# Performance work log

Measured on AMD Instinct MI355X. Metric: run time of the kernel, lower is better.

Reference implementation:

```python
import jax, jax.numpy as jnp
import numpy as np

B, N, M = 4, 2048, 2048
DIM, DIM_KEYS, DIM_OUT = 512, 512, 512
HEADS, DIM_HEAD = 8, 64
INNER = HEADS * DIM_HEAD


def setup_inputs() -> dict:
    key = jax.random.key(0)
    ks = jax.random.split(key, 8)
    x = jax.random.normal(ks[0], (B, N, DIM), dtype=jnp.float32)
    context = jax.random.normal(ks[1], (B, M, DIM_KEYS), dtype=jnp.float32)
    Wq = jax.random.normal(ks[2], (DIM, INNER), dtype=jnp.float32) / np.sqrt(DIM)
    Wkv = jax.random.normal(ks[3], (DIM_KEYS, 2 * INNER), dtype=jnp.float32) / np.sqrt(DIM_KEYS)
    null_k = jax.random.normal(ks[4], (DIM_HEAD,), dtype=jnp.float32)
    null_v = jax.random.normal(ks[5], (DIM_HEAD,), dtype=jnp.float32)
    Wout = jax.random.normal(ks[6], (INNER, DIM_OUT), dtype=jnp.float32) / np.sqrt(INNER)
    bout = jnp.zeros((DIM_OUT,), dtype=jnp.float32)
    return {"x": x, "context": context, "Wq": Wq, "Wkv": Wkv,
            "null_k": null_k, "null_v": null_v, "Wout": Wout, "bout": bout}


def reference(x, context, Wq, Wkv, null_k, null_v, Wout, bout):
    b = x.shape[0]
    scale = DIM_HEAD ** (-0.5)
    q = x @ Wq                      # [b, n, inner]
    kv = context @ Wkv              # [b, m, 2*inner]
    k, v = jnp.split(kv, 2, axis=-1)
    # [b, h, n, d]
    q = q.reshape(b, -1, HEADS, DIM_HEAD).transpose(0, 2, 1, 3)
    k = k.reshape(b, -1, HEADS, DIM_HEAD).transpose(0, 2, 1, 3)
    v = v.reshape(b, -1, HEADS, DIM_HEAD).transpose(0, 2, 1, 3)
    # prepend null key/value token: [b, h, 1, d]
    nk = jnp.broadcast_to(null_k, (b, HEADS, 1, DIM_HEAD))
    nv = jnp.broadcast_to(null_v, (b, HEADS, 1, DIM_HEAD))
    k = jnp.concatenate((nk, k), axis=-2)  # [b, h, m+1, d]
    v = jnp.concatenate((nv, v), axis=-2)
    q = jnp.tanh(q)
    k = jnp.tanh(k)
    sim = jnp.einsum('bhid,bhjd->bhij', q, k) * scale  # [b, h, n, m+1]
    attn = jax.nn.softmax(sim, axis=-1)
    out = jnp.einsum('bhij,bhjd->bhid', attn, v)       # [b, h, n, d]
    out = out.transpose(0, 2, 1, 3).reshape(b, -1, INNER)  # [b, n, inner]
    return out @ Wout + bout
```

## Files before the change

kernel.cpp:

```cpp
#include <hip/hip_runtime.h>
#include <hip/hip_bf16.h>
#include <stdint.h>

#define B_    4
#define N_    2048
#define M_    2048
#define DIMX  512
#define INNER 512
#define H_    8
#define DH    64
#define MK    2049
#define MKP   2112

#define QSCALE  0.18033688011f
#define SM_BIAS -11.5415605f

using u16 = unsigned short;
using u32 = unsigned int;

typedef __attribute__((ext_vector_type(8))) short short8;
typedef __attribute__((ext_vector_type(4))) float f32x4;

#if defined(__has_builtin)
# if __has_builtin(__builtin_amdgcn_exp2f)
#  define EXP2(x) __builtin_amdgcn_exp2f(x)
# endif
#endif
#ifndef EXP2
# define EXP2(x) exp2f(x)
#endif

__device__ __forceinline__ u16 bfc(float f){
  __hip_bfloat16 h = __float2bfloat16(f);
  return *reinterpret_cast<u16*>(&h);
}
__device__ __forceinline__ u32 bfpk(float lo, float hi){
  return (u32)bfc(lo) | ((u32)bfc(hi) << 16);
}
__device__ __forceinline__ u32 bfpk_tr(float lo, float hi){
  union { float f; u32 u; } a, b; a.f = lo; b.f = hi;
  return (a.u >> 16) | (b.u & 0xffff0000u);
}

__global__ __launch_bounds__(256) void prep(
    const float* __restrict__ x, const float* __restrict__ ctx,
    const float* __restrict__ Wq, const float* __restrict__ Wkv,
    const float* __restrict__ Wout,
    const float* __restrict__ nk, const float* __restrict__ nv,
    u16* __restrict__ xb, u16* __restrict__ cb,
    u16* __restrict__ Wqt, u16* __restrict__ Wkvt, u16* __restrict__ Woutt,
    u16* __restrict__ kb, u16* __restrict__ vt)
{
  const int bid = blockIdx.x;
  if (bid < 4096){
    const float* in = (bid < 2048) ? x : ctx;
    u16* out        = (bid < 2048) ? xb : cb;
    const int i = (bid & 2047) * 256 + threadIdx.x;
    float4 a = ((const float4*)in)[i*2];
    float4 b = ((const float4*)in)[i*2+1];
    uint4 t;
    t.x = bfpk(a.x, a.y); t.y = bfpk(a.z, a.w);
    t.z = bfpk(b.x, b.y); t.w = bfpk(b.z, b.w);
    ((uint4*)out)[i] = t;
    return;
  }
  if (bid >= 4480){
    const int i = (bid - 4480) * 256 + threadIdx.x;
    const int d = i & 63, bh = i >> 6;
    kb[((size_t)bh * MKP + 2048) * DH + d] = bfc(tanhf(nk[d]));
    vt[((size_t)bh * DH + d) * MKP + 2048] = bfc(nv[d]);
    return;
  }
  const int tt = bid - 4096;
  const int z  = tt >> 7;
  const int rem = tt & 127;
  const int cx = rem & 15, ry = rem >> 4;
  const float* in = (z == 0) ? Wq : (z == 1) ? Wkv : Wout;
  u16* out        = (z == 0) ? Wqt : (z == 1) ? Wkvt : Woutt;
  const int C     = (z == 1) ? 1024 : 512;
  const int R     = 512;
  if (cx * 64 >= C) return;

  __shared__ float tl[64][65];
  const int t = threadIdx.x;
  const int c0 = cx * 64, r0 = ry * 64;
  const int col = t & 63, rb = t >> 6;
  #pragma unroll
  for (int j = 0; j < 16; ++j){
    const int row = rb + j*4;
    tl[row][col] = in[(size_t)(r0 + row) * C + c0 + col];
  }
  __syncthreads();
  #pragma unroll
  for (int j = 0; j < 16; ++j){
    const int orow = rb + j*4;
    out[(size_t)(c0 + orow) * R + r0 + col] = bfc(tl[col][orow]);
  }
}

#define PROJ_COMPUTE(bi)                                                      \
  {                                                                           \
    short8 af[4], bf[4];                                                      \
    _Pragma("unroll")                                                         \
    for (int m = 0; m < 4; ++m){                                              \
      const int row = wr + m*16 + c;                                          \
      af[m] = *(const short8*)((char*)At[bi] + row*64 + ((g ^ ((row>>1)&3)) << 4)); \
    }                                                                         \
    _Pragma("unroll")                                                         \
    for (int n = 0; n < 4; ++n){                                              \
      const int row = wc + n*16 + c;                                          \
      bf[n] = *(const short8*)((char*)Bl[bi] + row*64 + ((g ^ ((row>>1)&3)) << 4)); \
    }                                                                         \
    __builtin_amdgcn_s_setprio(1);                                            \
    _Pragma("unroll")                                                         \
    for (int m = 0; m < 4; ++m)                                               \
      _Pragma("unroll")                                                       \
      for (int n = 0; n < 4; ++n)                                             \
        acc[m][n] = __builtin_amdgcn_mfma_f32_16x16x32_bf16(af[m], bf[n], acc[m][n], 0, 0, 0); \
    __builtin_amdgcn_s_setprio(0);                                            \
  }

__global__ __launch_bounds__(256, 3) void fused_proj(
    const u16* __restrict__ xb, const u16* __restrict__ cb,
    const u16* __restrict__ Wqt, const u16* __restrict__ Wkvt,
    u16* __restrict__ qb, u16* __restrict__ kb, u16* __restrict__ vt)
{
  __shared__ __align__(16) short At[2][128*32];
  __shared__ __align__(16) short Bl[2][128*32];

  const int flat = blockIdx.x;
  const int tile = (flat & 7) * 96 + (flat >> 3);
  const bool isq = tile < 256;
  const int lt   = isq ? tile : tile - 256;
  const int gx   = isq ? 4 : 8;
  const int row0 = (lt / gx) * 128, col0 = (lt % gx) * 128;
  const u16* A  = isq ? xb : cb;
  const u16* Bt = isq ? Wqt : Wkvt;

  const int tid = threadIdx.x;
  const int w = tid >> 6, lane = tid & 63;
  const int c = lane & 15, g = lane >> 4;
  const int wr = (w >> 1) * 64, wc = (w & 1) * 64;

  f32x4 acc[4][4] = {};

  const int srow = tid >> 1, sj = (tid & 1) * 2;
  const int swz0 = ((sj  ) ^ ((srow >> 1) & 3)) << 4;
  const int swz1 = ((sj+1) ^ ((srow >> 1) & 3)) << 4;

  const u16* asrc = A  + (size_t)(row0 + srow) * DIMX + sj*8;
  const u16* bsrc = Bt + (size_t)(col0 + srow) * DIMX + sj*8;

  uint4 aA0, aA1, bA0, bA1;
  uint4 aB0, aB1, bB0, bB1;

  aA0 = ((const uint4*)asrc)[0];        aA1 = ((const uint4*)asrc)[1];
  bA0 = ((const uint4*)bsrc)[0];        bA1 = ((const uint4*)bsrc)[1];
  aB0 = ((const uint4*)(asrc + 32))[0]; aB1 = ((const uint4*)(asrc + 32))[1];
  bB0 = ((const uint4*)(bsrc + 32))[0]; bB1 = ((const uint4*)(bsrc + 32))[1];
  *(uint4*)((char*)At[0] + srow*64 + swz0) = aA0;
  *(uint4*)((char*)At[0] + srow*64 + swz1) = aA1;
  *(uint4*)((char*)Bl[0] + srow*64 + swz0) = bA0;
  *(uint4*)((char*)Bl[0] + srow*64 + swz1) = bA1;

  for (int kk = 0; kk < 16; kk += 2){
    __syncthreads();
    if (kk + 2 < 16){
      const u16* an = asrc + (kk+2)*32;
      const u16* bn = bsrc + (kk+2)*32;
      aA0 = ((const uint4*)an)[0]; aA1 = ((const uint4*)an)[1];
      bA0 = ((const uint4*)bn)[0]; bA1 = ((const uint4*)bn)[1];
    }
    PROJ_COMPUTE(0);
    *(uint4*)((char*)At[1] + srow*64 + swz0) = aB0;
    *(uint4*)((char*)At[1] + srow*64 + swz1) = aB1;
    *(uint4*)((char*)Bl[1] + srow*64 + swz0) = bB0;
    *(uint4*)((char*)Bl[1] + srow*64 + swz1) = bB1;

    __syncthreads();
    if (kk + 3 < 16){
      const u16* an = asrc + (kk+3)*32;
      const u16* bn = bsrc + (kk+3)*32;
      aB0 = ((const uint4*)an)[0]; aB1 = ((const uint4*)an)[1];
      bB0 = ((const uint4*)bn)[0]; bB1 = ((const uint4*)bn)[1];
    }
    PROJ_COMPUTE(1);
    if (kk + 2 < 16){
      *(uint4*)((char*)At[0] + srow*64 + swz0) = aA0;
      *(uint4*)((char*)At[0] + srow*64 + swz1) = aA1;
      *(uint4*)((char*)Bl[0] + srow*64 + swz0) = bA0;
      *(uint4*)((char*)Bl[0] + srow*64 + swz1) = bA1;
    }
  }

  #pragma unroll
  for (int m = 0; m < 4; ++m){
    #pragma unroll
    for (int n = 0; n < 4; ++n){
      const int R0  = row0 + wr + m*16 + g*4;
      const int col = col0 + wc + n*16 + c;
      if (isq){
        #pragma unroll
        for (int rr = 0; rr < 4; ++rr)
          qb[(size_t)(R0 + rr) * INNER + col] = bfc(tanhf(acc[m][n][rr]) * QSCALE);
      } else {
        const int bidx = R0 >> 11, mm = R0 & 2047;
        if (col < INNER){
          const int h = col >> 6, d = col & 63;
          #pragma unroll
          for (int rr = 0; rr < 4; ++rr)
            kb[((size_t)(bidx*H_ + h) * MKP + mm + rr) * DH + d] =
                bfc(tanhf(acc[m][n][rr]));
        } else {
          const int cc = col - INNER;
          const int h = cc >> 6, d = cc & 63;
          uint2 o;
          o.x = bfpk(acc[m][n][0], acc[m][n][1]);
          o.y = bfpk(acc[m][n][2], acc[m][n][3]);
          *(uint2*)(vt + ((size_t)(bidx*H_ + h) * DH + d) * MKP + mm) = o;
        }
      }
    }
  }
}

__global__ __launch_bounds__(256, 3) void mgemm_out(
    const u16* __restrict__ A, const u16* __restrict__ Bt,
    float* __restrict__ Cf, const float* __restrict__ bias)
{
  __shared__ __align__(16) short At[2][128*32];
  __shared__ __align__(16) short Bl[2][64*32];

  const int flat = blockIdx.x;
  const int tile = (flat & 7) * 64 + (flat >> 3);
  const int row0 = (tile >> 3) * 128, col0 = (tile & 7) * 64;

  const int tid = threadIdx.x;
  const int w = tid >> 6, lane = tid & 63;
  const int c = lane & 15, g = lane >> 4;
  const int wr = (w >> 1) * 64, wc = (w & 1) * 32;

  f32x4 acc[4][2] = {};

  const int srow = tid >> 1, sj = (tid & 1) * 2;
  const int swz0 = ((sj  ) ^ ((srow >> 1) & 3)) << 4;
  const int swz1 = ((sj+1) ^ ((srow >> 1) & 3)) << 4;
  const int brow = tid >> 2, bch = tid & 3;
  const int bswz = (bch ^ ((brow >> 1) & 3)) << 4;

  const u16* asrc = A  + (size_t)(row0 + srow) * INNER + sj*8;
  const u16* bsrc = Bt + (size_t)(col0 + brow) * INNER + bch*8;

  uint4 aA0, aA1, bA0;
  uint4 aB0, aB1, bB0;

  aA0 = ((const uint4*)asrc)[0];        aA1 = ((const uint4*)asrc)[1];
  bA0 = *(const uint4*)bsrc;
  aB0 = ((const uint4*)(asrc + 32))[0]; aB1 = ((const uint4*)(asrc + 32))[1];
  bB0 = *(const uint4*)(bsrc + 32);
  *(uint4*)((char*)At[0] + srow*64 + swz0) = aA0;
  *(uint4*)((char*)At[0] + srow*64 + swz1) = aA1;
  *(uint4*)((char*)Bl[0] + brow*64 + bswz) = bA0;

  for (int kk = 0; kk < 16; kk += 2){
    __syncthreads();
    if (kk + 2 < 16){
      const u16* an = asrc + (kk+2)*32;
      aA0 = ((const uint4*)an)[0]; aA1 = ((const uint4*)an)[1];
      bA0 = *(const uint4*)(bsrc + (kk+2)*32);
    }
    {
      short8 af[4], bf[2];
      #pragma unroll
      for (int m = 0; m < 4; ++m){
        const int row = wr + m*16 + c;
        af[m] = *(const short8*)((char*)At[0] + row*64 + ((g ^ ((row>>1)&3)) << 4));
      }
      #pragma unroll
      for (int n = 0; n < 2; ++n){
        const int row = wc + n*16 + c;
        bf[n] = *(const short8*)((char*)Bl[0] + row*64 + ((g ^ ((row>>1)&3)) << 4));
      }
      __builtin_amdgcn_s_setprio(1);
      #pragma unroll
      for (int m = 0; m < 4; ++m)
        #pragma unroll
        for (int n = 0; n < 2; ++n)
          acc[m][n] = __builtin_amdgcn_mfma_f32_16x16x32_bf16(af[m], bf[n], acc[m][n], 0, 0, 0);
      __builtin_amdgcn_s_setprio(0);
    }
    *(uint4*)((char*)At[1] + srow*64 + swz0) = aB0;
    *(uint4*)((char*)At[1] + srow*64 + swz1) = aB1;
    *(uint4*)((char*)Bl[1] + brow*64 + bswz) = bB0;

    __syncthreads();
    if (kk + 3 < 16){
      const u16* an = asrc + (kk+3)*32;
      aB0 = ((const uint4*)an)[0]; aB1 = ((const uint4*)an)[1];
      bB0 = *(const uint4*)(bsrc + (kk+3)*32);
    }
    {
      short8 af[4], bf[2];
      #pragma unroll
      for (int m = 0; m < 4; ++m){
        const int row = wr + m*16 + c;
        af[m] = *(const short8*)((char*)At[1] + row*64 + ((g ^ ((row>>1)&3)) << 4));
      }
      #pragma unroll
      for (int n = 0; n < 2; ++n){
        const int row = wc + n*16 + c;
        bf[n] = *(const short8*)((char*)Bl[1] + row*64 + ((g ^ ((row>>1)&3)) << 4));
      }
      __builtin_amdgcn_s_setprio(1);
      #pragma unroll
      for (int m = 0; m < 4; ++m)
        #pragma unroll
        for (int n = 0; n < 2; ++n)
          acc[m][n] = __builtin_amdgcn_mfma_f32_16x16x32_bf16(af[m], bf[n], acc[m][n], 0, 0, 0);
      __builtin_amdgcn_s_setprio(0);
    }
    if (kk + 2 < 16){
      *(uint4*)((char*)At[0] + srow*64 + swz0) = aA0;
      *(uint4*)((char*)At[0] + srow*64 + swz1) = aA1;
      *(uint4*)((char*)Bl[0] + brow*64 + bswz) = bA0;
    }
  }

  #pragma unroll
  for (int m = 0; m < 4; ++m){
    #pragma unroll
    for (int n = 0; n < 2; ++n){
      #pragma unroll
      for (int rr = 0; rr < 4; ++rr){
        const int R = row0 + wr + m*16 + g*4 + rr;
        const int col = col0 + wc + n*16 + c;
        Cf[(size_t)R * 512 + col] = acc[m][n][rr] + bias[col];
      }
    }
  }
}

__global__ __launch_bounds__(256) void attn_mfma(
    const u16* __restrict__ qb, const u16* __restrict__ kb,
    const u16* __restrict__ vt, u16* __restrict__ aob)
{
  __shared__ __align__(16) short Kl[2][64*64];
  __shared__ __align__(16) short Vl[2][64*64];
  __shared__ __align__(16) short Pl[4][32*64];

  const int tid  = threadIdx.x;
  const int w    = tid >> 6;
  const int lane = tid & 63;
  const int c    = lane & 15;
  const int g    = lane >> 4;
  const int bh   = blockIdx.y, b = bh >> 3, h = bh & 7;
  const int qbase = blockIdx.x * 128 + w * 32;
  const int xr   = (c & 7) << 4;

  short8 qf[2][2];
  #pragma unroll
  for (int u = 0; u < 2; ++u){
    const u16* qrow = qb + ((size_t)(b*N_) + qbase + u*16 + c) * INNER + h * DH;
    qf[u][0] = *(const short8*)(qrow + g*8);
    qf[u][1] = *(const short8*)(qrow + 32 + g*8);
  }

  f32x4 o[2][4] = {};
  f32x4 lacc[2] = {};
  const short8 ones = {0x3F80,0x3F80,0x3F80,0x3F80,0x3F80,0x3F80,0x3F80,0x3F80};

  const u16* kbase = kb + (size_t)bh * MKP * DH;
  const u16* vbase = vt + (size_t)bh * DH * MKP;
  const int srow = tid >> 2, sch = (tid & 3) * 2;
  const int swz0 = ((sch  ) ^ (srow & 7)) << 4;
  const int swz1 = ((sch+1) ^ (srow & 7)) << 4;

  uint4 rk0, rk1, rv0, rv1;
  {
    const u16* ksrc = kbase + (size_t)srow * DH + sch*8;
    rk0 = ((const uint4*)ksrc)[0]; rk1 = ((const uint4*)ksrc)[1];
    const u16* vsrc = vbase + (size_t)srow * MKP + sch*8;
    rv0 = ((const uint4*)vsrc)[0]; rv1 = ((const uint4*)vsrc)[1];
  }
  *(uint4*)((char*)Kl[0] + srow*128 + swz0) = rk0;
  *(uint4*)((char*)Kl[0] + srow*128 + swz1) = rk1;
  *(uint4*)((char*)Vl[0] + srow*128 + swz0) = rv0;
  *(uint4*)((char*)Vl[0] + srow*128 + swz1) = rv1;

  int cur = 0;
  for (int kt = 0; kt < 33; ++kt){
    __syncthreads();
    if (kt < 32){
      const u16* ksrc = kbase + (size_t)((kt+1)*64 + srow) * DH + sch*8;
      rk0 = ((const uint4*)ksrc)[0]; rk1 = ((const uint4*)ksrc)[1];
      const u16* vsrc = vbase + (size_t)srow * MKP + (kt+1)*64 + sch*8;
      rv0 = ((const uint4*)vsrc)[0]; rv1 = ((const uint4*)vsrc)[1];
    }

    const char* Kc = (const char*)Kl[cur];
    const char* Vc = (const char*)Vl[cur];
    char*       Pw = (char*)Pl + w*4096;

    f32x4 sv[2][4];
    __builtin_amdgcn_s_setprio(1);
    #pragma unroll
    for (int s = 0; s < 4; ++s){
      const int row = s*16 + c;
      short8 kf0 = *(const short8*)(Kc + row*128 + ((     g*16) ^ xr));
      short8 kf1 = *(const short8*)(Kc + row*128 + ((64 + g*16) ^ xr));
      f32x4 a0 = {SM_BIAS, SM_BIAS, SM_BIAS, SM_BIAS};
      f32x4 a1 = {SM_BIAS, SM_BIAS, SM_BIAS, SM_BIAS};
      a0 = __builtin_amdgcn_mfma_f32_16x16x32_bf16(kf0, qf[0][0], a0, 0, 0, 0);
      a1 = __builtin_amdgcn_mfma_f32_16x16x32_bf16(kf0, qf[1][0], a1, 0, 0, 0);
      a0 = __builtin_amdgcn_mfma_f32_16x16x32_bf16(kf1, qf[0][1], a0, 0, 0, 0);
      a1 = __builtin_amdgcn_mfma_f32_16x16x32_bf16(kf1, qf[1][1], a1, 0, 0, 0);
      sv[0][s] = a0; sv[1][s] = a1;
    }
    __builtin_amdgcn_s_setprio(0);

    if (kt == 32){
      #pragma unroll
      for (int u = 0; u < 2; ++u)
        #pragma unroll
        for (int s = 0; s < 4; ++s)
          #pragma unroll
          for (int r = 0; r < 4; ++r)
            if (s | r) sv[u][s][r] = -1e30f;
      if (g){ sv[0][0][0] = -1e30f; sv[1][0][0] = -1e30f; }
    }

    #pragma unroll
    for (int u = 0; u < 2; ++u){
      #pragma unroll
      for (int s = 0; s < 4; ++s){
        const float p0 = EXP2(sv[u][s][0]);
        const float p1 = EXP2(sv[u][s][1]);
        const float p2 = EXP2(sv[u][s][2]);
        const float p3 = EXP2(sv[u][s][3]);
        uint2 pk;
        pk.x = bfpk_tr(p0, p1);
        pk.y = bfpk_tr(p2, p3);
        *(uint2*)(Pw + (u*16 + c)*128
                  + ((((2*s + (g>>1)) ^ (c&7)) << 4) | ((g&1)*8))) = pk;
      }
    }

    __builtin_amdgcn_s_setprio(1);
    #pragma unroll
    for (int hh = 0; hh < 2; ++hh){
      short8 pf0 = *(const short8*)(Pw + (     c)*128 + (((hh*4 + g) ^ (c&7)) << 4));
      short8 pf1 = *(const short8*)(Pw + (16 + c)*128 + (((hh*4 + g) ^ (c&7)) << 4));
      lacc[0] = __builtin_amdgcn_mfma_f32_16x16x32_bf16(pf0, ones, lacc[0], 0, 0, 0);
      lacc[1] = __builtin_amdgcn_mfma_f32_16x16x32_bf16(pf1, ones, lacc[1], 0, 0, 0);
      #pragma unroll
      for (int D = 0; D < 4; ++D){
        short8 vf = *(const short8*)(Vc + (D*16 + c)*128 + ((hh*64 + g*16) ^ xr));
        o[0][D] = __builtin_amdgcn_mfma_f32_16x16x32_bf16(pf0, vf, o[0][D], 0, 0, 0);
        o[1][D] = __builtin_amdgcn_mfma_f32_16x16x32_bf16(pf1, vf, o[1][D], 0, 0, 0);
      }
    }
    __builtin_amdgcn_s_setprio(0);

    if (kt < 32){
      char* Kn = (char*)Kl[cur ^ 1];
      char* Vn = (char*)Vl[cur ^ 1];
      *(uint4*)(Kn + srow*128 + swz0) = rk0;
      *(uint4*)(Kn + srow*128 + swz1) = rk1;
      *(uint4*)(Vn + srow*128 + swz0) = rv0;
      *(uint4*)(Vn + srow*128 + swz1) = rv1;
      cur ^= 1;
    }
  }

  #pragma unroll
  for (int u = 0; u < 2; ++u){
    #pragma unroll
    for (int r = 0; r < 4; ++r){
      const float ir = 1.f / lacc[u][r];
      const size_t nrow = (size_t)(b*N_) + qbase + u*16 + g*4 + r;
      #pragma unroll
      for (int D = 0; D < 4; ++D)
        aob[nrow * INNER + h*DH + D*16 + c] = bfc(o[u][D][r] * ir);
    }
  }
}

extern "C" void kernel_launch(void* const* d_in, const int* in_sizes, int n_in,
                              void* d_out, int out_size, void* d_ws, size_t ws_size,
                              hipStream_t stream)
{
  const float* x    = (const float*)d_in[0];
  const float* ctx  = (const float*)d_in[1];
  const float* Wq   = (const float*)d_in[2];
  const float* Wkv  = (const float*)d_in[3];
  const float* nk   = (const float*)d_in[4];
  const float* nv   = (const float*)d_in[5];
  const float* Wout = (const float*)d_in[6];
  const float* bout = (const float*)d_in[7];
  float* out = (float*)d_out;

  char* ws = (char*)d_ws;
  u16* xb    = (u16*)(ws);
  u16* cb    = (u16*)(ws +  8388608);
  u16* qb    = (u16*)(ws + 16777216);
  u16* kbB   = (u16*)(ws + 25165824);
  u16* vtb   = (u16*)(ws + 33816576);
  u16* Wqt   = (u16*)(ws + 42467328);
  u16* Wkvt  = (u16*)(ws + 42991616);
  u16* Woutt = (u16*)(ws + 44040192);
  u16* aoB   = xb;

  prep<<<4488, 256, 0, stream>>>(x, ctx, Wq, Wkv, Wout, nk, nv,
                                 xb, cb, Wqt, Wkvt, Woutt, kbB, vtb);

  fused_proj<<<768, 256, 0, stream>>>(xb, cb, Wqt, Wkvt, qb, kbB, vtb);
  attn_mfma<<<dim3(16, 32), 256, 0, stream>>>(qb, kbB, vtb, aoB);
  mgemm_out<<<512, 256, 0, stream>>>(aoB, Woutt, out, bout);
}
```

Before: 101.1 us.

## Stage K/V tiles with direct global-to-LDS loads using pre-swizzled layouts

The attention kernel's K/V tile staging moves from global loads into registers followed by swizzled LDS stores to direct global_load_lds (buffer-to-LDS) transfers. This frees registers and removes the LDS store instructions from the loop. Because the direct loads cannot swizzle on the fly, the projection GEMM epilogue and the null-token prep now write K and V^T to global memory in the XOR-swizzled order the LDS reads expect. The risk is that the wait/sync semantics for asynchronous LDS loads are handled only by the existing __syncthreads, and the scattered swizzled global writes may coalesce less well.

```diff
diff --git a/kernel.cpp b/kernel.cpp
--- a/kernel.cpp
+++ b/kernel.cpp
@@ -40,6 +40,12 @@
 __device__ __forceinline__ u32 bfpk_tr(float lo, float hi){
   union { float f; u32 u; } a, b; a.f = lo; b.f = hi;
   return (a.u >> 16) | (b.u & 0xffff0000u);
+}
+
+__device__ __forceinline__ void gload16(const void* g, void* l){
+  __builtin_amdgcn_global_load_lds(
+      (const __attribute__((address_space(1))) unsigned int*)g,
+      (__attribute__((address_space(3))) unsigned int*)l, 16, 0, 0);
 }
 
 __global__ __launch_bounds__(256) void prep(
@@ -68,7 +74,7 @@
     const int i = (bid - 4480) * 256 + threadIdx.x;
     const int d = i & 63, bh = i >> 6;
     kb[((size_t)bh * MKP + 2048) * DH + d] = bfc(tanhf(nk[d]));
-    vt[((size_t)bh * DH + d) * MKP + 2048] = bfc(nv[d]);
+    vt[((size_t)bh * DH + d) * MKP + 2048 + ((d & 7) << 3)] = bfc(nv[d]);
     return;
   }
   const int tt = bid - 4096;
@@ -208,16 +214,22 @@
         if (col < INNER){
           const int h = col >> 6, d = col & 63;
           #pragma unroll
-          for (int rr = 0; rr < 4; ++rr)
-            kb[((size_t)(bidx*H_ + h) * MKP + mm + rr) * DH + d] =
+          for (int rr = 0; rr < 4; ++rr){
+            const int key = mm + rr;
+            const int dsw = (((d >> 3) ^ (key & 7)) << 3) | (d & 7);
+            kb[((size_t)(bidx*H_ + h) * MKP + key) * DH + dsw] =
                 bfc(tanhf(acc[m][n][rr]));
+          }
         } else {
           const int cc = col - INNER;
           const int h = cc >> 6, d = cc & 63;
+          const int tb = mm & ~63;
+          const int sl = ((mm & 63) >> 3) ^ (d & 7);
           uint2 o;
           o.x = bfpk(acc[m][n][0], acc[m][n][1]);
           o.y = bfpk(acc[m][n][2], acc[m][n][3]);
-          *(uint2*)(vt + ((size_t)(bidx*H_ + h) * DH + d) * MKP + mm) = o;
+          *(uint2*)(vt + ((size_t)(bidx*H_ + h) * DH + d) * MKP
+                    + tb + (sl << 3) + (mm & 7)) = o;
         }
       }
     }
@@ -371,31 +383,25 @@
 
   const u16* kbase = kb + (size_t)bh * MKP * DH;
   const u16* vbase = vt + (size_t)bh * DH * MKP;
-  const int srow = tid >> 2, sch = (tid & 3) * 2;
-  const int swz0 = ((sch  ) ^ (srow & 7)) << 4;
-  const int swz1 = ((sch+1) ^ (srow & 7)) << 4;
-
-  uint4 rk0, rk1, rv0, rv1;
-  {
-    const u16* ksrc = kbase + (size_t)srow * DH + sch*8;
-    rk0 = ((const uint4*)ksrc)[0]; rk1 = ((const uint4*)ksrc)[1];
-    const u16* vsrc = vbase + (size_t)srow * MKP + sch*8;
-    rv0 = ((const uint4*)vsrc)[0]; rv1 = ((const uint4*)vsrc)[1];
-  }
-  *(uint4*)((char*)Kl[0] + srow*128 + swz0) = rk0;
-  *(uint4*)((char*)Kl[0] + srow*128 + swz1) = rk1;
-  *(uint4*)((char*)Vl[0] + srow*128 + swz0) = rv0;
-  *(uint4*)((char*)Vl[0] + srow*128 + swz1) = rv1;
+  const int srw = w*8 + (lane >> 3);
+  const int sck = (lane & 7) * 8;
+
+  #define STAGE(buf, kt)                                                       \
+    gload16(kbase + (size_t)((kt)*64 +      srw) * DH + sck,                   \
+            (char*)Kl[buf] +        w*1024);                                   \
+    gload16(kbase + (size_t)((kt)*64 + 32 + srw) * DH + sck,                   \
+            (char*)Kl[buf] + 4096 + w*1024);                                   \
+    gload16(vbase + (size_t)(     srw) * MKP + (kt)*64 + sck,                  \
+            (char*)Vl[buf] +        w*1024);                                   \
+    gload16(vbase + (size_t)(32 + srw) * MKP + (kt)*64 + sck,                  \
+            (char*)Vl[buf] + 4096 + w*1024);
+
+  STAGE(0, 0);
 
   int cur = 0;
   for (int kt = 0; kt < 33; ++kt){
     __syncthreads();
-    if (kt < 32){
-      const u16* ksrc = kbase + (size_t)((kt+1)*64 + srow) * DH + sch*8;
-      rk0 = ((const uint4*)ksrc)[0]; rk1 = ((const uint4*)ksrc)[1];
-      const u16* vsrc = vbase + (size_t)srow * MKP + (kt+1)*64 + sch*8;
-      rv0 = ((const uint4*)vsrc)[0]; rv1 = ((const uint4*)vsrc)[1];
-    }
+    if (kt < 32){ STAGE(cur ^ 1, kt + 1); }
 
     const char* Kc = (const char*)Kl[cur];
     const char* Vc = (const char*)Vl[cur];
@@ -461,15 +467,7 @@
     }
     __builtin_amdgcn_s_setprio(0);
 
-    if (kt < 32){
-      char* Kn = (char*)Kl[cur ^ 1];
-      char* Vn = (char*)Vl[cur ^ 1];
-      *(uint4*)(Kn + srow*128 + swz0) = rk0;
-      *(uint4*)(Kn + srow*128 + swz1) = rk1;
-      *(uint4*)(Vn + srow*128 + swz0) = rv0;
-      *(uint4*)(Vn + srow*128 + swz1) = rv1;
-      cur ^= 1;
-    }
+    if (kt < 32) cur ^= 1;
   }
 
   #pragma unroll
```

After: 103.6 us. +2.5%, slower.
